# Optimization experiments

Measured on AMD Instinct MI355X. Metric: run time of the kernel, lower is better.

Reference implementation:

```python
import jax, jax.numpy as jnp
import numpy as np

NA = 100_000   # authors
NP = 100_000   # papers
E = 1_600_000  # edges per edge type (avg degree 16)
DD, DC = 32, 32
H = 64
OUT = 16
L = 2


def setup_inputs() -> dict:
    key = jax.random.key(0)
    ks = jax.random.split(key, 32)
    n = lambda i, shape, s: jax.random.normal(ks[i], shape, dtype=jnp.float32) * s
    ri = lambda i, shape, hi: jax.random.randint(ks[i], shape, 0, hi, dtype=jnp.int32)
    w = 0.1  # weight scale
    return {
        "x_d_author": n(0, (NA, DD), 1.0),
        "x_c_author": n(1, (NA, DC), 1.0),
        "x_d_paper": n(2, (NP, DD), 1.0),
        "x_c_paper": n(3, (NP, DC), 1.0),
        "win_author_w": n(4, (DD + DC, H), w),
        "win_author_b": n(5, (H,), w),
        "win_paper_w": n(6, (DD + DC, H), w),
        "win_paper_b": n(7, (H,), w),
        "writes_wl": n(8, (L, H, H), w),
        "writes_bl": n(9, (L, H), w),
        "writes_wr": n(10, (L, H, H), w),
        "wb_wl": n(11, (L, H, H), w),
        "wb_bl": n(12, (L, H), w),
        "wb_wr": n(13, (L, H, H), w),
        "cites_wl": n(14, (L, H, H), w),
        "cites_bl": n(15, (L, H), w),
        "cites_wr": n(16, (L, H, H), w),
        "lin_w": n(17, (H, OUT), w),
        "lin_b": n(18, (OUT,), w),
        "writes_src": ri(19, (E,), NA),  # author -> paper
        "writes_dst": ri(20, (E,), NP),
        "wb_src": ri(21, (E,), NP),      # paper -> author
        "wb_dst": ri(22, (E,), NA),
        "cites_src": ri(23, (E,), NP),   # paper -> paper
        "cites_dst": ri(24, (E,), NP),
    }


def _sage(x_src, x_dst, src, dst, n_dst, wl, bl, wr):
    # SAGEConv: lin_l(mean_{j in N(i)} x_j) + lin_r(x_i); zero-degree nodes get 0 aggregate.
    agg = jax.ops.segment_sum(x_src[src], dst, num_segments=n_dst)       # [n_dst, H]
    cnt = jax.ops.segment_sum(jnp.ones_like(dst, jnp.float32), dst, num_segments=n_dst)
    mean = agg / jnp.maximum(cnt, 1.0)[:, None]
    return mean @ wl + bl + x_dst @ wr


def reference(x_d_author, x_c_author, x_d_paper, x_c_paper,
              win_author_w, win_author_b, win_paper_w, win_paper_b,
              writes_wl, writes_bl, writes_wr,
              wb_wl, wb_bl, wb_wr,
              cites_wl, cites_bl, cites_wr,
              lin_w, lin_b,
              writes_src, writes_dst, wb_src, wb_dst, cites_src, cites_dst):
    # per-node-type input projection + relu
    y_a = jax.nn.relu(jnp.concatenate([x_d_author, x_c_author], axis=1) @ win_author_w + win_author_b)
    y_p = jax.nn.relu(jnp.concatenate([x_d_paper, x_c_paper], axis=1) @ win_paper_w + win_paper_b)
    # heterogeneous SAGE layers; HeteroConv sums edge-type outputs per dst node type
    for l in range(L):
        new_p = (_sage(y_a, y_p, writes_src, writes_dst, NP, writes_wl[l], writes_bl[l], writes_wr[l])
                 + _sage(y_p, y_p, cites_src, cites_dst, NP, cites_wl[l], cites_bl[l], cites_wr[l]))
        new_a = _sage(y_p, y_a, wb_src, wb_dst, NA, wb_wl[l], wb_bl[l], wb_wr[l])
        y_a, y_p = new_a, new_p
    return y_p @ lin_w + lin_b  # [NP, OUT]
```

## Files before the change

kernel.cpp:

```cpp
#include <hip/hip_runtime.h>
#include <hip/hip_fp16.h>

#define NNODE 100000
#define NEDGE 1600000
#define NBUCK 196
#define BSH 9
#define PCH 8192
#define CAP 9216

typedef _Float16 f16x8 __attribute__((ext_vector_type(8)));
typedef float f32x4 __attribute__((ext_vector_type(4)));


__global__ __launch_bounds__(512) void partition_kernel(
    const int* __restrict__ s0, const int* __restrict__ s1, const int* __restrict__ s2,
    const int* __restrict__ d0, const int* __restrict__ d1, const int* __restrict__ d2,
    int* __restrict__ bc, int* __restrict__ pairs) {
    int y = blockIdx.y;
    const int* src = (y == 0) ? s0 : (y == 1) ? s1 : s2;
    const int* dst = (y == 0) ? d0 : (y == 1) ? d1 : d2;
    int* bcur = bc + y * 256;
    int* pr = pairs + (size_t)y * (NBUCK * CAP);

    __shared__ int sCur[NBUCK];
    __shared__ int sDelta[NBUCK];
    __shared__ int sScan[256];
    __shared__ int sSort[PCH];
    __shared__ unsigned char sBid[PCH];
    int t = threadIdx.x;
    for (int i = t; i < NBUCK; i += 512) sCur[i] = 0;
    __syncthreads();
    int c0 = blockIdx.x * PCH;
    int cend = min(c0 + PCH, NEDGE);
    int nblk = cend - c0;
    for (int e = c0 + t; e < cend; e += 512)
        atomicAdd(&sCur[dst[e] >> BSH], 1);
    __syncthreads();
    int v = (t < NBUCK) ? sCur[t] : 0;
    if (t < 256) sScan[t] = v;
    __syncthreads();
    for (int off = 1; off < 256; off <<= 1) {
        int a = (t < 256) ? sScan[t] : 0;
        int b = (t >= off && t < 256) ? sScan[t - off] : 0;
        __syncthreads();
        if (t < 256) sScan[t] = a + b;
        __syncthreads();
    }
    if (t < NBUCK) {
        int excl = sScan[t] - v;
        sCur[t] = excl;
        int gb = v ? atomicAdd(&bcur[t], v) : 0;
        sDelta[t] = gb - excl;
    }
    __syncthreads();
    for (int e = c0 + t; e < cend; e += 512) {
        int d = dst[e];
        int b = d >> BSH;
        int slot = atomicAdd(&sCur[b], 1);
        sSort[slot] = ((d & 511) << 17) | src[e];
        sBid[slot] = (unsigned char)b;
    }
    __syncthreads();
    for (int i = t; i < nblk; i += 512)
        pr[sDelta[sBid[i]] + i] = sSort[i];
}

__global__ __launch_bounds__(512) void bucket_csr_kernel(const int* __restrict__ bc,
                                                         const int* __restrict__ pairs,
                                                         int2* __restrict__ rowptr2,
                                                         int* __restrict__ ssrc) {
    int y = blockIdx.y;
    pairs += (size_t)y * (NBUCK * CAP);
    rowptr2 += (size_t)y * NNODE;
    ssrc += (size_t)y * (NBUCK * CAP);

    __shared__ int sIn[CAP];
    __shared__ int sOut[CAP];
    __shared__ int cnt[512];
    __shared__ int cur[512];
    __shared__ int s1[512];
    int b = blockIdx.x;
    int t = threadIdx.x;
    int node0 = b << BSH;
    int start = b * CAP;
    int end = bc[y * 256 + b];
    int m = end - start;

    cnt[t] = 0;
    __syncthreads();
    for (int i = t; i < m; i += 512) {
        int p = pairs[start + i];
        sIn[i] = p;
        atomicAdd(&cnt[p >> 17], 1);
    }
    __syncthreads();
    int v = cnt[t];
    s1[t] = v;
    __syncthreads();
    for (int off = 1; off < 512; off <<= 1) {
        int a = s1[t];
        int c = (t >= off) ? s1[t - off] : 0;
        __syncthreads();
        s1[t] = a + c;
        __syncthreads();
    }
    int eb = s1[t] - v;
    cur[t] = eb;
    if (node0 + t < NNODE) rowptr2[node0 + t] = make_int2(start + eb, start + eb + v);
    __syncthreads();
    for (int i = t; i < m; i += 512) {
        int p = sIn[i];
        int pos = atomicAdd(&cur[p >> 17], 1);
        sOut[pos] = p & 0x1FFFF;
    }
    __syncthreads();
    for (int i = t; i < m; i += 512)
        ssrc[start + i] = sOut[i];
}

__device__ __forceinline__ void gather_body(const __half* __restrict__ x,
                                            const int2* __restrict__ rowptr2,
                                            const int* __restrict__ ssrc,
                                            __half* __restrict__ out) {
    int wid = (blockIdx.x * 256 + threadIdx.x) >> 6;
    int lane = threadIdx.x & 63;
    if (wid >= NNODE) return;
    int ee = lane >> 3;
    int fo = (lane & 7) << 3;
    int2 se = rowptr2[wid];
    int start = se.x, end = se.y;
    int deg = end - start;
    int nfull = deg >> 4;
    __half2 h0 = __float2half2_rn(0.f), h1 = h0, h2 = h0, h3 = h0;
    for (int w = 0; w < nfull; ++w) {
        int e = start + (w << 4) + ee;
        int v0 = ssrc[e], v1 = ssrc[e + 8];
        uint4 r0 = *(const uint4*)(x + ((size_t)v0 << 6) + fo);
        uint4 r1 = *(const uint4*)(x + ((size_t)v1 << 6) + fo);
        h0 = __hadd2(h0, *(__half2*)&r0.x);
        h1 = __hadd2(h1, *(__half2*)&r0.y);
        h2 = __hadd2(h2, *(__half2*)&r0.z);
        h3 = __hadd2(h3, *(__half2*)&r0.w);
        h0 = __hadd2(h0, *(__half2*)&r1.x);
        h1 = __hadd2(h1, *(__half2*)&r1.y);
        h2 = __hadd2(h2, *(__half2*)&r1.z);
        h3 = __hadd2(h3, *(__half2*)&r1.w);
    }
    __half2 one = __float2half2_rn(1.f), zero = __float2half2_rn(0.f);
    for (int e0 = start + (nfull << 4); e0 < end; e0 += 8) {
        int ea = e0 + ee;
        bool pa = ea < end;
        int ia = pa ? ea : start;
        int va = ssrc[ia];
        uint4 ra = *(const uint4*)(x + ((size_t)va << 6) + fo);
        __half2 hm = pa ? one : zero;
        h0 = __hfma2(hm, *(__half2*)&ra.x, h0);
        h1 = __hfma2(hm, *(__half2*)&ra.y, h1);
        h2 = __hfma2(hm, *(__half2*)&ra.z, h2);
        h3 = __hfma2(hm, *(__half2*)&ra.w, h3);
    }
#define RED8(hh) { \
        int u_ = *(int*)&hh; int r_; \
        r_ = __shfl_xor(u_, 8);  hh = __hadd2(hh, *(__half2*)&r_); u_ = *(int*)&hh; \
        r_ = __shfl_xor(u_, 16); hh = __hadd2(hh, *(__half2*)&r_); u_ = *(int*)&hh; \
        r_ = __shfl_xor(u_, 32); hh = __hadd2(hh, *(__half2*)&r_); }
    RED8(h0) RED8(h1) RED8(h2) RED8(h3)
#undef RED8
    if (ee == 0) {
        float scale = 1.0f / fmaxf((float)deg, 1.0f);
        float2 f0 = __half22float2(h0), f1 = __half22float2(h1);
        float2 f2 = __half22float2(h2), f3 = __half22float2(h3);
        uint4 w;
        *(__half2*)&w.x = __floats2half2_rn(f0.x * scale, f0.y * scale);
        *(__half2*)&w.y = __floats2half2_rn(f1.x * scale, f1.y * scale);
        *(__half2*)&w.z = __floats2half2_rn(f2.x * scale, f2.y * scale);
        *(__half2*)&w.w = __floats2half2_rn(f3.x * scale, f3.y * scale);
        *(uint4*)(out + ((size_t)wid << 6) + fo) = w;
    }
}

__global__ __launch_bounds__(256) void gather3_kernel(
    const __half* __restrict__ x0, const __half* __restrict__ x1, const __half* __restrict__ x2,
    const int2* __restrict__ rp0, const int2* __restrict__ rp1, const int2* __restrict__ rp2,
    const int* __restrict__ ss0, const int* __restrict__ ss1, const int* __restrict__ ss2,
    __half* __restrict__ o0, __half* __restrict__ o1, __half* __restrict__ o2) {
    int y = blockIdx.y;
    if (y == 0) gather_body(x0, rp0, ss0, o0);
    else if (y == 1) gather_body(x1, rp1, ss1, o1);
    else gather_body(x2, rp2, ss2, o2);
}

__global__ __launch_bounds__(256) void gather2_kernel(
    const __half* __restrict__ x0, const __half* __restrict__ x1,
    const int2* __restrict__ rp0, const int2* __restrict__ rp1,
    const int* __restrict__ ss0, const int* __restrict__ ss1,
    __half* __restrict__ o0, __half* __restrict__ o1) {
    int y = blockIdx.y;
    if (y == 0) gather_body(x0, rp0, ss0, o0);
    else gather_body(x1, rp1, ss1, o1);
}

__global__ __launch_bounds__(256) void wprep_kernel(
    const float* __restrict__ writes_wl, const float* __restrict__ cites_wl,
    const float* __restrict__ writes_wr, const float* __restrict__ cites_wr,
    const float* __restrict__ wb_wl, const float* __restrict__ wb_wr,
    const float* __restrict__ winA_w, const float* __restrict__ winP_w,
    const float* __restrict__ lin_w,
    const float* __restrict__ writes_bl, const float* __restrict__ cites_bl,
    __half* __restrict__ wtP0, __half* __restrict__ wtP1, __half* __restrict__ wtA,
    __half* __restrict__ wtPJA, __half* __restrict__ wtPJP, __half* __restrict__ wtLIN,
    float* __restrict__ biasP, int* __restrict__ bcur) {
    int i = blockIdx.x * 256 + threadIdx.x;
    if (i < 24576) {
        int l = i / 12288, j = i % 12288;
        int n = j / 192, k = j % 192;
        float v;
        if (k < 64) v = writes_wl[l * 4096 + k * 64 + n];
        else if (k < 128) v = cites_wl[l * 4096 + (k - 64) * 64 + n];
        else v = writes_wr[l * 4096 + (k - 128) * 64 + n] +
                 cites_wr[l * 4096 + (k - 128) * 64 + n];
        (l ? wtP1 : wtP0)[n * 192 + k] = __float2half(v);
    } else if (i < 32768) {
        int j = i - 24576;
        int n = j / 128, k = j % 128;
        float v = (k < 64) ? wb_wl[k * 64 + n] : wb_wr[(k - 64) * 64 + n];
        wtA[n * 128 + k] = __float2half(v);
    } else if (i < 36864) {
        int j = i - 32768;
        wtPJA[j] = __float2half(winA_w[(j % 64) * 64 + j / 64]);
    } else if (i < 40960) {
        int j = i - 36864;
        wtPJP[j] = __float2half(winP_w[(j % 64) * 64 + j / 64]);
    } else if (i < 41984) {
        int j = i - 40960;
        wtLIN[j] = __float2half(lin_w[(j % 64) * 16 + j / 64]);
    } else if (i < 42112) {
        int j = i - 41984;
        biasP[j] = writes_bl[j] + cites_bl[j];
    } else if (i < 42880) {
        int j = i - 42112;
        bcur[j] = (j & 255) * CAP;
    }
}

__device__ inline f16x8 cvt8(const float* p) {
    float4 a = *(const float4*)p, b = *(const float4*)(p + 4);
    f16x8 r;
    r[0] = (_Float16)a.x; r[1] = (_Float16)a.y; r[2] = (_Float16)a.z; r[3] = (_Float16)a.w;
    r[4] = (_Float16)b.x; r[5] = (_Float16)b.y; r[6] = (_Float16)b.z; r[7] = (_Float16)b.w;
    return r;
}

__global__ __launch_bounds__(256) void proj_mfma(const float* __restrict__ xd0,
                                                 const float* __restrict__ xc0,
                                                 const float* __restrict__ xd1,
                                                 const float* __restrict__ xc1,
                                                 const __half* __restrict__ wt0,
                                                 const __half* __restrict__ wt1,
                                                 const float* __restrict__ b0,
                                                 const float* __restrict__ b1,
                                                 __half* __restrict__ o0,
                                                 __half* __restrict__ o1) {
    int yb = blockIdx.y;
    const float* xd = yb ? xd1 : xd0;
    const float* xc = yb ? xc1 : xc0;
    const __half* wt = yb ? wt1 : wt0;
    const float* bias = yb ? b1 : b0;
    __half* out = yb ? o1 : o0;
    int wid = (blockIdx.x * 256 + threadIdx.x) >> 6;
    if (wid >= NNODE / 16) return;
    int lane = threadIdx.x & 63;
    int row = lane & 15, kq = lane >> 4;
    int node0 = wid << 4;
    f16x8 af0 = cvt8(xd + (size_t)(node0 + row) * 32 + kq * 8);
    f16x8 af1 = cvt8(xc + (size_t)(node0 + row) * 32 + kq * 8);
#pragma unroll
    for (int nt = 0; nt < 4; ++nt) {
        int col = nt * 16 + row;
        const __half* wp = wt + (size_t)col * 64 + kq * 8;
        f32x4 acc = {0.f, 0.f, 0.f, 0.f};
        acc = __builtin_amdgcn_mfma_f32_16x16x32_f16(af0, *(const f16x8*)(wp), acc, 0, 0, 0);
        acc = __builtin_amdgcn_mfma_f32_16x16x32_f16(af1, *(const f16x8*)(wp + 32), acc, 0, 0, 0);
        float b = bias[col];
#pragma unroll
        for (int r = 0; r < 4; ++r)
            out[((size_t)(node0 + kq * 4 + r) << 6) + col] = __float2half(fmaxf(acc[r] + b, 0.f));
    }
}

template <int NSEG>
__device__ __forceinline__ void combine_body(const __half* __restrict__ a0,
                                             const __half* __restrict__ a1,
                                             const __half* __restrict__ a2,
                                             const __half* __restrict__ wt,
                                             const float* __restrict__ bias,
                                             __half* __restrict__ out) {
    int wid = (blockIdx.x * 256 + threadIdx.x) >> 6;
    if (wid >= NNODE / 16) return;
    int lane = threadIdx.x & 63;
    int row = lane & 15, kq = lane >> 4;
    int node0 = wid << 4;
    const int K = NSEG * 64;
    const __half* as[3] = {a0, a1, a2};
    f16x8 af[2 * NSEG];
#pragma unroll
    for (int s = 0; s < NSEG; ++s) {
        const __half* p = as[s] + ((size_t)(node0 + row) << 6) + kq * 8;
        af[2 * s] = *(const f16x8*)(p);
        af[2 * s + 1] = *(const f16x8*)(p + 32);
    }
#pragma unroll
    for (int nt = 0; nt < 4; ++nt) {
        int col = nt * 16 + row;
        const __half* wp = wt + (size_t)col * K + kq * 8;
        f32x4 acc = {0.f, 0.f, 0.f, 0.f};
#pragma unroll
        for (int t = 0; t < 2 * NSEG; ++t)
            acc = __builtin_amdgcn_mfma_f32_16x16x32_f16(af[t], *(const f16x8*)(wp + t * 32), acc, 0, 0, 0);
        float b = bias[col];
#pragma unroll
        for (int r = 0; r < 4; ++r)
            out[((size_t)(node0 + kq * 4 + r) << 6) + col] = __float2half(acc[r] + b);
    }
}

__global__ __launch_bounds__(256) void combine_dual(
    const __half* __restrict__ pm0, const __half* __restrict__ pm1, const __half* __restrict__ py,
    const __half* __restrict__ am0, const __half* __restrict__ ay,
    const __half* __restrict__ wtP, const __half* __restrict__ wtA,
    const float* __restrict__ bP, const float* __restrict__ bA,
    __half* __restrict__ oP, __half* __restrict__ oA) {
    if (blockIdx.y == 0) combine_body<3>(pm0, pm1, py, wtP, bP, oP);
    else combine_body<2>(am0, ay, nullptr, wtA, bA, oA);
}

__global__ __launch_bounds__(256) void combine3_kernel(const __half* __restrict__ a0,
                                                       const __half* __restrict__ a1,
                                                       const __half* __restrict__ a2,
                                                       const __half* __restrict__ wt,
                                                       const float* __restrict__ bias,
                                                       __half* __restrict__ out) {
    combine_body<3>(a0, a1, a2, wt, bias, out);
}

__global__ __launch_bounds__(256) void final_mfma(const __half* __restrict__ y,
                                                  const __half* __restrict__ wt,
                                                  const float* __restrict__ bias,
                                                  float* __restrict__ out) {
    int wid = (blockIdx.x * 256 + threadIdx.x) >> 6;
    if (wid >= NNODE / 16) return;
    int lane = threadIdx.x & 63;
    int row = lane & 15, kq = lane >> 4;
    int node0 = wid << 4;
    const __half* p = y + ((size_t)(node0 + row) << 6) + kq * 8;
    f16x8 af0 = *(const f16x8*)(p);
    f16x8 af1 = *(const f16x8*)(p + 32);
    const __half* wp = wt + (size_t)row * 64 + kq * 8;
    f32x4 acc = {0.f, 0.f, 0.f, 0.f};
    acc = __builtin_amdgcn_mfma_f32_16x16x32_f16(af0, *(const f16x8*)(wp), acc, 0, 0, 0);
    acc = __builtin_amdgcn_mfma_f32_16x16x32_f16(af1, *(const f16x8*)(wp + 32), acc, 0, 0, 0);
    float b = bias[row];
#pragma unroll
    for (int r = 0; r < 4; ++r)
        out[(size_t)(node0 + kq * 4 + r) * 16 + row] = acc[r] + b;
}

extern "C" void kernel_launch(void* const* d_in, const int* in_sizes, int n_in,
                              void* d_out, int out_size, void* d_ws, size_t ws_size,
                              hipStream_t stream) {
    (void)in_sizes; (void)n_in; (void)out_size; (void)ws_size;
    const float* xda = (const float*)d_in[0];
    const float* xca = (const float*)d_in[1];
    const float* xdp = (const float*)d_in[2];
    const float* xcp = (const float*)d_in[3];
    const float* winA_w = (const float*)d_in[4];
    const float* winA_b = (const float*)d_in[5];
    const float* winP_w = (const float*)d_in[6];
    const float* winP_b = (const float*)d_in[7];
    const float* writes_wl = (const float*)d_in[8];
    const float* writes_bl = (const float*)d_in[9];
    const float* writes_wr = (const float*)d_in[10];
    const float* wb_wl = (const float*)d_in[11];
    const float* wb_bl = (const float*)d_in[12];
    const float* wb_wr = (const float*)d_in[13];
    const float* cites_wl = (const float*)d_in[14];
    const float* cites_bl = (const float*)d_in[15];
    const float* cites_wr = (const float*)d_in[16];
    const float* lin_w = (const float*)d_in[17];
    const float* lin_b = (const float*)d_in[18];
    const int* w_src = (const int*)d_in[19];
    const int* w_dst = (const int*)d_in[20];
    const int* b_src = (const int*)d_in[21];
    const int* b_dst = (const int*)d_in[22];
    const int* c_src = (const int*)d_in[23];
    const int* c_dst = (const int*)d_in[24];

    const size_t NF = (size_t)NNODE * 64;
    const size_t BUK = (size_t)NBUCK * CAP;
    __half* B0 = (__half*)d_ws;
    __half* B1 = B0 + NF;
    __half* B2 = B1 + NF;
    __half* B3 = B2 + NF;
    __half* B4 = B3 + NF;

    __half* wtP0 = B4 + NF;
    __half* wtP1 = wtP0 + 12288;
    __half* wtA = wtP1 + 12288;
    __half* wtPJA = wtA + 8192;
    __half* wtPJP = wtPJA + 4096;
    __half* wtLIN = wtPJP + 4096;
    float* biasP = (float*)(wtLIN + 1024);

    int* ip = (int*)(biasP + 128);
    int2* rp2 = (int2*)ip;
    int* bcur = (int*)(rp2 + 3 * NNODE);
    int* ssrc = bcur + 3 * 256;
    int* pairs = (int*)B2;

    const int GB = (NNODE * 64) / 256;
    const int MB = (NNODE / 16 + 3) / 4;
    const int PB = (NEDGE + PCH - 1) / PCH;

    wprep_kernel<<<168, 256, 0, stream>>>(writes_wl, cites_wl, writes_wr, cites_wr,
                                          wb_wl, wb_wr, winA_w, winP_w, lin_w,
                                          writes_bl, cites_bl,
                                          wtP0, wtP1, wtA, wtPJA, wtPJP, wtLIN, biasP, bcur);
    partition_kernel<<<dim3(PB, 3), 512, 0, stream>>>(w_src, c_src, b_src,
                                                      w_dst, c_dst, b_dst, bcur, pairs);
    bucket_csr_kernel<<<dim3(NBUCK, 3), 512, 0, stream>>>(bcur, pairs, rp2, ssrc);

    const int2* rp_w = rp2;
    const int2* rp_c = rp2 + NNODE;
    const int2* rp_b = rp2 + 2 * NNODE;
    const int* ss_w = ssrc;
    const int* ss_c = ssrc + BUK;
    const int* ss_b = ssrc + 2 * BUK;

    proj_mfma<<<dim3(MB, 2), 256, 0, stream>>>(xda, xca, xdp, xcp,
                                               wtPJA, wtPJP, winA_b, winP_b, B0, B1);

    gather3_kernel<<<dim3(GB, 3), 256, 0, stream>>>(B0, B1, B1,
                                                    rp_w, rp_c, rp_b,
                                                    ss_w, ss_c, ss_b,
                                                    B2, B3, B4);
    combine_dual<<<dim3(MB, 2), 256, 0, stream>>>(B2, B3, B1, B4, B0,
                                                  wtP0, wtA, biasP, wb_bl, B2, B4);

    gather2_kernel<<<dim3(GB, 2), 256, 0, stream>>>(B4, B2,
                                                    rp_w, rp_c,
                                                    ss_w, ss_c,
                                                    B0, B1);
    combine3_kernel<<<MB, 256, 0, stream>>>(B0, B1, B2, wtP1, biasP + 64, B0);

    final_mfma<<<MB, 256, 0, stream>>>(B0, wtLIN, lin_b, (float*)d_out);
}
```

Before: 314.9 us.

## Fuse last combine with output linear, privatize partition histograms, use 32-bit gather offsets

Merges the final layer's combine and the output projection into one kernel that keeps the 16x64 tile in LDS, so the intermediate paper embedding never round-trips through global memory and one launch is dropped. The partition histogram now uses four per-wavegroup LDS copies to cut atomic contention. Gather address math switches to unsigned 32-bit offsets to save 64-bit integer instructions. These add LDS use in the fused kernel and rely on offsets fitting in 32 bits.

```diff
diff --git a/kernel.cpp b/kernel.cpp
--- a/kernel.cpp
+++ b/kernel.cpp
@@ -22,21 +22,24 @@
     int* bcur = bc + y * 256;
     int* pr = pairs + (size_t)y * (NBUCK * CAP);
 
+    __shared__ int sCnt4[4][NBUCK];
     __shared__ int sCur[NBUCK];
     __shared__ int sDelta[NBUCK];
     __shared__ int sScan[256];
     __shared__ int sSort[PCH];
     __shared__ unsigned char sBid[PCH];
     int t = threadIdx.x;
-    for (int i = t; i < NBUCK; i += 512) sCur[i] = 0;
+    for (int i = t; i < 4 * NBUCK; i += 512) sCnt4[0][i] = 0;
     __syncthreads();
     int c0 = blockIdx.x * PCH;
     int cend = min(c0 + PCH, NEDGE);
     int nblk = cend - c0;
+    int* myCnt = sCnt4[(t >> 7) & 3];
     for (int e = c0 + t; e < cend; e += 512)
-        atomicAdd(&sCur[dst[e] >> BSH], 1);
-    __syncthreads();
-    int v = (t < NBUCK) ? sCur[t] : 0;
+        atomicAdd(&myCnt[dst[e] >> BSH], 1);
+    __syncthreads();
+    int v = 0;
+    if (t < NBUCK) v = sCnt4[0][t] + sCnt4[1][t] + sCnt4[2][t] + sCnt4[3][t];
     if (t < 256) sScan[t] = v;
     __syncthreads();
     for (int off = 1; off < 256; off <<= 1) {
@@ -126,7 +129,7 @@
     int lane = threadIdx.x & 63;
     if (wid >= NNODE) return;
     int ee = lane >> 3;
-    int fo = (lane & 7) << 3;
+    unsigned fo = (lane & 7) << 3;
     int2 se = rowptr2[wid];
     int start = se.x, end = se.y;
     int deg = end - start;
@@ -134,9 +137,9 @@
     __half2 h0 = __float2half2_rn(0.f), h1 = h0, h2 = h0, h3 = h0;
     for (int w = 0; w < nfull; ++w) {
         int e = start + (w << 4) + ee;
-        int v0 = ssrc[e], v1 = ssrc[e + 8];
-        uint4 r0 = *(const uint4*)(x + ((size_t)v0 << 6) + fo);
-        uint4 r1 = *(const uint4*)(x + ((size_t)v1 << 6) + fo);
+        unsigned v0 = (unsigned)ssrc[e], v1 = (unsigned)ssrc[e + 8];
+        uint4 r0 = *(const uint4*)(x + ((v0 << 6) + fo));
+        uint4 r1 = *(const uint4*)(x + ((v1 << 6) + fo));
         h0 = __hadd2(h0, *(__half2*)&r0.x);
         h1 = __hadd2(h1, *(__half2*)&r0.y);
         h2 = __hadd2(h2, *(__half2*)&r0.z);
@@ -151,8 +154,8 @@
         int ea = e0 + ee;
         bool pa = ea < end;
         int ia = pa ? ea : start;
-        int va = ssrc[ia];
-        uint4 ra = *(const uint4*)(x + ((size_t)va << 6) + fo);
+        unsigned va = (unsigned)ssrc[ia];
+        uint4 ra = *(const uint4*)(x + ((va << 6) + fo));
         __half2 hm = pa ? one : zero;
         h0 = __hfma2(hm, *(__half2*)&ra.x, h0);
         h1 = __hfma2(hm, *(__half2*)&ra.y, h1);
@@ -175,7 +178,7 @@
         *(__half2*)&w.y = __floats2half2_rn(f1.x * scale, f1.y * scale);
         *(__half2*)&w.z = __floats2half2_rn(f2.x * scale, f2.y * scale);
         *(__half2*)&w.w = __floats2half2_rn(f3.x * scale, f3.y * scale);
-        *(uint4*)(out + ((size_t)wid << 6) + fo) = w;
+        *(uint4*)(out + (((unsigned)wid << 6) + fo)) = w;
     }
 }
 
@@ -334,32 +337,46 @@
     else combine_body<2>(am0, ay, nullptr, wtA, bA, oA);
 }
 
-__global__ __launch_bounds__(256) void combine3_kernel(const __half* __restrict__ a0,
-                                                       const __half* __restrict__ a1,
-                                                       const __half* __restrict__ a2,
-                                                       const __half* __restrict__ wt,
-                                                       const float* __restrict__ bias,
-                                                       __half* __restrict__ out) {
-    combine_body<3>(a0, a1, a2, wt, bias, out);
-}
-
-__global__ __launch_bounds__(256) void final_mfma(const __half* __restrict__ y,
-                                                  const __half* __restrict__ wt,
-                                                  const float* __restrict__ bias,
-                                                  float* __restrict__ out) {
+__global__ __launch_bounds__(256) void combine3_final_kernel(
+    const __half* __restrict__ a0, const __half* __restrict__ a1, const __half* __restrict__ a2,
+    const __half* __restrict__ wt, const float* __restrict__ bias,
+    const __half* __restrict__ wtLIN, const float* __restrict__ linb,
+    float* __restrict__ out) {
+    __shared__ __half sTile[4][16][64];
     int wid = (blockIdx.x * 256 + threadIdx.x) >> 6;
     if (wid >= NNODE / 16) return;
+    int wv = (threadIdx.x >> 6) & 3;
     int lane = threadIdx.x & 63;
     int row = lane & 15, kq = lane >> 4;
     int node0 = wid << 4;
-    const __half* p = y + ((size_t)(node0 + row) << 6) + kq * 8;
-    f16x8 af0 = *(const f16x8*)(p);
-    f16x8 af1 = *(const f16x8*)(p + 32);
-    const __half* wp = wt + (size_t)row * 64 + kq * 8;
+    const __half* as[3] = {a0, a1, a2};
+    f16x8 af[6];
+#pragma unroll
+    for (int s = 0; s < 3; ++s) {
+        const __half* p = as[s] + ((size_t)(node0 + row) << 6) + kq * 8;
+        af[2 * s] = *(const f16x8*)(p);
+        af[2 * s + 1] = *(const f16x8*)(p + 32);
+    }
+#pragma unroll
+    for (int nt = 0; nt < 4; ++nt) {
+        int col = nt * 16 + row;
+        const __half* wp = wt + (size_t)col * 192 + kq * 8;
+        f32x4 acc = {0.f, 0.f, 0.f, 0.f};
+#pragma unroll
+        for (int t = 0; t < 6; ++t)
+            acc = __builtin_amdgcn_mfma_f32_16x16x32_f16(af[t], *(const f16x8*)(wp + t * 32), acc, 0, 0, 0);
+        float b = bias[col];
+#pragma unroll
+        for (int r = 0; r < 4; ++r)
+            sTile[wv][kq * 4 + r][col] = __float2half(acc[r] + b);
+    }
+    f16x8 y0 = *(const f16x8*)(&sTile[wv][row][kq * 8]);
+    f16x8 y1 = *(const f16x8*)(&sTile[wv][row][kq * 8 + 32]);
+    const __half* wl = wtLIN + (size_t)row * 64 + kq * 8;
     f32x4 acc = {0.f, 0.f, 0.f, 0.f};
-    acc = __builtin_amdgcn_mfma_f32_16x16x32_f16(af0, *(const f16x8*)(wp), acc, 0, 0, 0);
-    acc = __builtin_amdgcn_mfma_f32_16x16x32_f16(af1, *(const f16x8*)(wp + 32), acc, 0, 0, 0);
-    float b = bias[row];
+    acc = __builtin_amdgcn_mfma_f32_16x16x32_f16(y0, *(const f16x8*)(wl), acc, 0, 0, 0);
+    acc = __builtin_amdgcn_mfma_f32_16x16x32_f16(y1, *(const f16x8*)(wl + 32), acc, 0, 0, 0);
+    float b = linb[row];
 #pragma unroll
     for (int r = 0; r < 4; ++r)
         out[(size_t)(node0 + kq * 4 + r) * 16 + row] = acc[r] + b;
@@ -450,7 +467,6 @@
                                                     rp_w, rp_c,
                                                     ss_w, ss_c,
                                                     B0, B1);
-    combine3_kernel<<<MB, 256, 0, stream>>>(B0, B1, B2, wtP1, biasP + 64, B0);
-
-    final_mfma<<<MB, 256, 0, stream>>>(B0, wtLIN, lin_b, (float*)d_out);
-}
+    combine3_final_kernel<<<MB, 256, 0, stream>>>(B0, B1, B2, wtP1, biasP + 64,
+                                                  wtLIN, lin_b, (float*)d_out);
+}
```

After: 309.6 us. Within noise of the previous version (-1.7%).
